# Kernel tuning notes

Hardware: AMD Instinct MI355X
Metric: run time of the kernel (lower is better)

The kernel has to match this reference:

```python
import jax, jax.numpy as jnp
import numpy as np

HID = 100

def _make_params(key):
    dims = [(2, HID), (HID, HID), (HID, HID), (HID, HID), (HID, 2)]
    params = {}
    for i, (fan_in, fan_out) in enumerate(dims):
        k1, k2, key = jax.random.split(key, 3)
        bound = 1.0 / np.sqrt(fan_in)
        params[f"W{i+1}"] = jax.random.uniform(k1, (fan_out, fan_in), jnp.float32, -bound, bound)
        params[f"b{i+1}"] = jax.random.uniform(k2, (fan_out,), jnp.float32, -bound, bound)
    return params

def setup_inputs() -> dict:
    key = jax.random.key(0)
    kx, kt, kp = jax.random.split(key, 3)
    N = 262144
    inp = {
        "x": jax.random.normal(kx, (N, 1), jnp.float32),
        "t": jax.random.uniform(kt, (N, 1), jnp.float32),
    }
    inp.update(_make_params(kp))
    return inp

def reference(x, t, W1, b1, W2, b2, W3, b3, W4, b4, W5, b5):
    hidden = [(W1, b1), (W2, b2), (W3, b3), (W4, b4)]

    def u(xs, ts):  # scalar xs, ts -> [2] = (u_r, u_i)
        h = jnp.stack([xs, ts])
        for W, b in hidden:
            h = jnp.tanh(W @ h + b)
        return W5 @ h + b5

    u_t = jax.jacfwd(u, argnums=1)          # [2]: (u_t_r, u_t_i)
    u_x = jax.jacfwd(u, argnums=0)          # [2]
    u_xx = jax.jacfwd(u_x, argnums=0)       # [2]: (u_xx_r, u_xx_i)

    def per_point(xs, ts):
        return u(xs, ts), u_t(xs, ts), u_xx(xs, ts)

    U, Ut, Uxx = jax.vmap(per_point)(x[:, 0], t[:, 0])  # each [N, 2]

    u_r, u_i = U[:, 0:1], U[:, 1:2]
    u_t_r, u_t_i = Ut[:, 0:1], Ut[:, 1:2]
    u_xx_r, u_xx_i = Uxx[:, 0:1], Uxx[:, 1:2]

    mag2 = u_r * u_r + u_i * u_i
    f_r = -u_t_i + 0.5 * u_xx_r + mag2 * u_r
    f_i = u_t_r + 0.5 * u_xx_i + mag2 * u_i
    return f_r, f_i
```

## Files before the change

### kernel.cpp

```cpp
#include <hip/hip_runtime.h>


using half8 = __attribute__((ext_vector_type(8))) _Float16;
using half4 = __attribute__((ext_vector_type(4))) _Float16;
using f32x4 = __attribute__((ext_vector_type(4))) float;

#define LW      44800
#define ZOFF    134400
#define STGOFF  134416
#define STGW    2304
#define PLANEB  1152
#define SMEM_BYTES 152848

union U8 { uint4 u; half8 h; };
union U4 { uint2 u; half4 h; };

static __device__ __forceinline__ float fast_tanh(float z) {
    float e = __expf(2.0f * z);
    return 1.0f - 2.0f * __builtin_amdgcn_rcpf(e + 1.0f);
}

static __device__ __forceinline__ void split2(float v, _Float16& h0, _Float16& h1) {
    h0 = (_Float16)v;
    h1 = (_Float16)((v - (float)h0) * 512.0f);
}

__global__ void prep_w(const float* __restrict__ W2, const float* __restrict__ W3,
                       const float* __restrict__ W4, unsigned short* __restrict__ ws) {
    int bid = blockIdx.x;
    int l = bid / 28, rem = bid % 28, kt = rem / 7, jt = rem % 7;
    const float* W = (l == 0) ? W2 : (l == 1) ? W3 : W4;
    int lane = threadIdx.x;
    int c = lane & 15, q = lane >> 4;
    int j = 16 * jt + c;
    if (kt < 3) {
        for (int s = 0; s < 2; ++s)
            for (int i = 0; i < 8; ++i) {
                int k = 32 * kt + 8 * q + i;
                float w = (j < 100) ? W[j * 100 + k] : 0.0f;
                _Float16 h0 = (_Float16)w;
                _Float16 val = (s == 0) ? h0 : (_Float16)((w - (float)h0) * 512.0f);
                ws[(l*LW + kt*14336 + jt*2048 + s*1024 + lane*16 + i*2) >> 1] =
                    __builtin_bit_cast(unsigned short, val);
            }
    } else if (lane < 16) {
        for (int s = 0; s < 2; ++s)
            for (int i = 0; i < 4; ++i) {
                int k = 96 + i;
                float w = (j < 100) ? W[j * 100 + k] : 0.0f;
                _Float16 h0 = (_Float16)w;
                _Float16 val = (s == 0) ? h0 : (_Float16)((w - (float)h0) * 512.0f);
                ws[(l*LW + 43008 + jt*256 + s*128 + lane*8 + i*2) >> 1] =
                    __builtin_bit_cast(unsigned short, val);
            }
    }
}

__global__ void __launch_bounds__(512, 2) pinn_mfma(
    const float* __restrict__ x,  const float* __restrict__ t,
    const float* __restrict__ W1, const float* __restrict__ b1,
    const float* __restrict__ b2, const float* __restrict__ b3,
    const float* __restrict__ b4,
    const float* __restrict__ W5, const float* __restrict__ b5,
    const char* __restrict__ ws, float* __restrict__ out,
    int N, int nchunks)
{
    extern __shared__ char smem[];
    const int tid  = threadIdx.x;
    const int w    = tid >> 6;
    const int lane = tid & 63;
    const int c15  = lane & 15;
    const int q    = lane >> 4;

    for (int it = 0; it < 17; ++it) {
        int idx = tid + it * 512;
        if (idx < 8400) ((uint4*)smem)[idx] = ((const uint4*)ws)[idx];
    }
    if (tid < 4) *(unsigned*)(smem + ZOFF + tid * 4) = 0u;
    __syncthreads();

    char* stg = smem + STGOFF + w * STGW;

    half8 a0[3], a1[3];
    half4 a0t,   a1t;
    f32x4 c0[7], c1[7];

    for (int chunk = blockIdx.x; chunk < nchunks; chunk += gridDim.x) {
        const int colbase = chunk * 128 + w * 16;

        {
            int col = colbase + c15;
            int pt = col >> 2, ch = col & 3;
            float xv = x[pt], tv = t[pt];
            #pragma unroll
            for (int kt = 0; kt < 3; ++kt) {
                half8 v0, v1;
                #pragma unroll
                for (int i = 0; i < 8; ++i) {
                    int j = 32 * kt + 8 * q + i;
                    float w0 = W1[2*j], w1 = W1[2*j+1], bb = b1[j];
                    float p = fmaf(w0, xv, fmaf(w1, tv, bb));
                    float a = fast_tanh(p);
                    float s = 1.0f - a * a;
                    float v = (ch == 0) ? a : (ch == 1) ? s * w1
                             : (ch == 2) ? s * w0 : -2.0f * a * s * w0 * w0;
                    _Float16 h0, h1; split2(v, h0, h1);
                    v0[i] = h0; v1[i] = h1;
                }
                a0[kt] = v0; a1[kt] = v1;
            }
            half4 t0 = {0, 0, 0, 0}, t1 = {0, 0, 0, 0};
            if (q == 0) {
                #pragma unroll
                for (int i = 0; i < 4; ++i) {
                    int j = 96 + i;
                    float w0 = W1[2*j], w1 = W1[2*j+1], bb = b1[j];
                    float p = fmaf(w0, xv, fmaf(w1, tv, bb));
                    float a = fast_tanh(p);
                    float s = 1.0f - a * a;
                    float v = (ch == 0) ? a : (ch == 1) ? s * w1
                             : (ch == 2) ? s * w0 : -2.0f * a * s * w0 * w0;
                    _Float16 h0, h1; split2(v, h0, h1);
                    t0[i] = h0; t1[i] = h1;
                }
            }
            a0t = t0; a1t = t1;
        }

        for (int l = 0; l < 3; ++l) {
            const char* WL = smem + l * LW;
            const float* BL = (l == 0) ? b2 : (l == 1) ? b3 : b4;

            #pragma unroll
            for (int jt = 0; jt < 7; ++jt) {
                c0[jt] = (f32x4){0.f, 0.f, 0.f, 0.f};
                c1[jt] = (f32x4){0.f, 0.f, 0.f, 0.f};
            }

            #pragma unroll
            for (int kt = 0; kt < 3; ++kt)
                #pragma unroll
                for (int jt = 0; jt < 7; ++jt) {
                    U8 b0u, b1u;
                    b0u.u = *(const uint4*)(WL + kt*14336 + jt*2048 + lane*16);
                    b1u.u = *(const uint4*)(WL + kt*14336 + jt*2048 + 1024 + lane*16);
                    c0[jt] = __builtin_amdgcn_mfma_f32_16x16x32_f16(a0[kt], b0u.h, c0[jt], 0, 0, 0);
                    c1[jt] = __builtin_amdgcn_mfma_f32_16x16x32_f16(a0[kt], b1u.h, c1[jt], 0, 0, 0);
                    c1[jt] = __builtin_amdgcn_mfma_f32_16x16x32_f16(a1[kt], b0u.h, c1[jt], 0, 0, 0);
                }
            #pragma unroll
            for (int jt = 0; jt < 7; ++jt) {
                int toff  = (lane < 16) ? (l*LW + 43008 + jt*256 + lane*8) : ZOFF;
                int toff1 = (lane < 16) ? (toff + 128) : ZOFF;
                U4 b0u, b1u;
                b0u.u = *(const uint2*)(smem + toff);
                b1u.u = *(const uint2*)(smem + toff1);
                c0[jt] = __builtin_amdgcn_mfma_f32_16x16x16f16(a0t, b0u.h, c0[jt], 0, 0, 0);
                c1[jt] = __builtin_amdgcn_mfma_f32_16x16x16f16(a0t, b1u.h, c1[jt], 0, 0, 0);
                c1[jt] = __builtin_amdgcn_mfma_f32_16x16x16f16(a1t, b0u.h, c1[jt], 0, 0, 0);
            }

            if (l < 2) {
                #pragma unroll
                for (int kc = 0; kc < 4; ++kc) {
                    int njt = (kc < 3) ? 2 : 1;
                    #pragma unroll
                    for (int jj = 0; jj < 2; ++jj) {
                        if (jj >= njt) continue;
                        int jt = 2 * kc + jj;
                        int kk = 16 * jj + c15;
                        int j  = 16 * jt + c15;
                        float bj = BL[(j < 100) ? j : 99];
                        float z0 = c0[jt][0] + c1[jt][0] * (1.0f/512.0f) + bj;
                        float z1 = c0[jt][1] + c1[jt][1] * (1.0f/512.0f);
                        float z2 = c0[jt][2] + c1[jt][2] * (1.0f/512.0f);
                        float z3 = c0[jt][3] + c1[jt][3] * (1.0f/512.0f);
                        float a = fast_tanh(z0);
                        float s = 1.0f - a * a;
                        float v[4];
                        v[0] = a; v[1] = s * z1; v[2] = s * z2;
                        v[3] = fmaf(-2.0f * a * s * z2, z2, s * z3);
                        #pragma unroll
                        for (int r = 0; r < 4; ++r) {
                            _Float16 h0, h1; split2(v[r], h0, h1);
                            _Float16* bp = (_Float16*)(stg) + (4 * q + r) * 36 + kk;
                            bp[0]   = h0;
                            bp[576] = h1;
                        }
                    }
                    if (kc < 3) {
                        const char* rb = stg + c15 * 72 + 16 * q;
                        U8 u;
                        uint2 L, H;
                        L = *(const uint2*)(rb);              H = *(const uint2*)(rb + 8);
                        u.u = (uint4){L.x, L.y, H.x, H.y};    a0[kc] = u.h;
                        L = *(const uint2*)(rb + PLANEB);     H = *(const uint2*)(rb + PLANEB + 8);
                        u.u = (uint4){L.x, L.y, H.x, H.y};    a1[kc] = u.h;
                    } else {
                        U4 u;
                        if (q == 0) {
                            const char* rb = stg + c15 * 72;
                            u.u = *(const uint2*)(rb);            a0t = u.h;
                            u.u = *(const uint2*)(rb + PLANEB);   a1t = u.h;
                        } else {
                            a0t = (half4){0,0,0,0}; a1t = (half4){0,0,0,0};
                        }
                    }
                }
            } else {
                float p00 = 0.f, p01 = 0.f, p03 = 0.f;
                float p10 = 0.f, p11 = 0.f, p13 = 0.f;
                #pragma unroll
                for (int jt = 0; jt < 7; ++jt) {
                    int j = 16 * jt + c15;
                    int j2 = (j < 100) ? j : 99;
                    float m = (j < 100) ? 1.0f : 0.0f;
                    float bj = BL[j2];
                    float w50 = W5[j2] * m, w51 = W5[100 + j2] * m;
                    float z0 = c0[jt][0] + c1[jt][0] * (1.0f/512.0f) + bj;
                    float z1 = c0[jt][1] + c1[jt][1] * (1.0f/512.0f);
                    float z2 = c0[jt][2] + c1[jt][2] * (1.0f/512.0f);
                    float z3 = c0[jt][3] + c1[jt][3] * (1.0f/512.0f);
                    float a = fast_tanh(z0);
                    float s = 1.0f - a * a;
                    float v0 = a, v1 = s * z1;
                    float v3 = fmaf(-2.0f * a * s * z2, z2, s * z3);
                    p00 = fmaf(w50, v0, p00);
                    p01 = fmaf(w50, v1, p01);
                    p03 = fmaf(w50, v3, p03);
                    p10 = fmaf(w51, v0, p10);
                    p11 = fmaf(w51, v1, p11);
                    p13 = fmaf(w51, v3, p13);
                }
                #pragma unroll
                for (int m = 1; m <= 8; m <<= 1) {
                    p00 += __shfl_xor(p00, m, 64);
                    p01 += __shfl_xor(p01, m, 64);
                    p03 += __shfl_xor(p03, m, 64);
                    p10 += __shfl_xor(p10, m, 64);
                    p11 += __shfl_xor(p11, m, 64);
                    p13 += __shfl_xor(p13, m, 64);
                }
                if (c15 == 0) {
                    float ur = p00 + b5[0], ui = p10 + b5[1];
                    float mag2 = ur * ur + ui * ui;
                    float fr = fmaf(mag2, ur, fmaf(0.5f, p03, -p11));
                    float fi = fmaf(mag2, ui, fmaf(0.5f, p13,  p01));
                    int pt = chunk * 32 + w * 4 + q;
                    out[pt]     = fr;
                    out[N + pt] = fi;
                }
            }
        }
    }
}

extern "C" void kernel_launch(void* const* d_in, const int* in_sizes, int n_in,
                              void* d_out, int out_size, void* d_ws, size_t ws_size,
                              hipStream_t stream) {
    const float* x  = (const float*)d_in[0];
    const float* t  = (const float*)d_in[1];
    const float* W1 = (const float*)d_in[2];
    const float* b1 = (const float*)d_in[3];
    const float* W2 = (const float*)d_in[4];
    const float* b2 = (const float*)d_in[5];
    const float* W3 = (const float*)d_in[6];
    const float* b3 = (const float*)d_in[7];
    const float* W4 = (const float*)d_in[8];
    const float* b4 = (const float*)d_in[9];
    const float* W5 = (const float*)d_in[10];
    const float* b5 = (const float*)d_in[11];
    float* out = (float*)d_out;
    const int N = in_sizes[0];
    const int nchunks = N / 32;

    (void)hipFuncSetAttribute((const void*)pinn_mfma,
                              hipFuncAttributeMaxDynamicSharedMemorySize, SMEM_BYTES);

    prep_w<<<84, 64, 0, stream>>>(W2, W3, W4, (unsigned short*)d_ws);
    pinn_mfma<<<256, 512, SMEM_BYTES, stream>>>(x, t, W1, b1, b2, b3, b4, W5, b5,
                                                (const char*)d_ws, out, N, nchunks);
}
```

Measured before the change: 465.7 us.

## Process two M-tiles per wave to reuse LDS weight fragments across MFMAs

Each wave now handles 32 columns (two 16-column M tiles) per chunk instead of 16, so each B-fragment loaded from LDS feeds twice as many MFMAs. The staging buffer row stride grows from 36 to 40 halves, which allows single 16-byte LDS reads in place of paired 8-byte reads. Chunk count halves and bounds guards are added for partial chunks. The cost is doubled accumulator and A-fragment register pressure, which may reduce occupancy or cause spills.

```diff
diff --git a/kernel.cpp b/kernel.cpp
--- a/kernel.cpp
+++ b/kernel.cpp
@@ -8,9 +8,9 @@
 #define LW      44800
 #define ZOFF    134400
 #define STGOFF  134416
-#define STGW    2304
-#define PLANEB  1152
-#define SMEM_BYTES 152848
+#define STGW    2560
+#define PLANEB  1280
+#define SMEM_BYTES 154896
 
 union U8 { uint4 u; half8 h; };
 union U4 { uint2 u; half4 h; };
@@ -81,17 +81,19 @@
 
     char* stg = smem + STGOFF + w * STGW;
 
-    half8 a0[3], a1[3];
-    half4 a0t,   a1t;
-    f32x4 c0[7], c1[7];
+    half8 a0[2][3], a1[2][3];
+    half4 a0t[2],   a1t[2];
+    f32x4 c0[7][2], c1[7][2];
 
     for (int chunk = blockIdx.x; chunk < nchunks; chunk += gridDim.x) {
-        const int colbase = chunk * 128 + w * 16;
-
-        {
-            int col = colbase + c15;
+        const int colbase = chunk * 256 + w * 32;
+
+        #pragma unroll
+        for (int mt = 0; mt < 2; ++mt) {
+            int col = colbase + 16 * mt + c15;
             int pt = col >> 2, ch = col & 3;
-            float xv = x[pt], tv = t[pt];
+            int ptc = (pt < N) ? pt : (N - 1);
+            float xv = x[ptc], tv = t[ptc];
             #pragma unroll
             for (int kt = 0; kt < 3; ++kt) {
                 half8 v0, v1;
@@ -107,7 +109,7 @@
                     _Float16 h0, h1; split2(v, h0, h1);
                     v0[i] = h0; v1[i] = h1;
                 }
-                a0[kt] = v0; a1[kt] = v1;
+                a0[mt][kt] = v0; a1[mt][kt] = v1;
             }
             half4 t0 = {0, 0, 0, 0}, t1 = {0, 0, 0, 0};
             if (q == 0) {
@@ -124,7 +126,7 @@
                     t0[i] = h0; t1[i] = h1;
                 }
             }
-            a0t = t0; a1t = t1;
+            a0t[mt] = t0; a1t[mt] = t1;
         }
 
         for (int l = 0; l < 3; ++l) {
@@ -132,10 +134,12 @@
             const float* BL = (l == 0) ? b2 : (l == 1) ? b3 : b4;
 
             #pragma unroll
-            for (int jt = 0; jt < 7; ++jt) {
-                c0[jt] = (f32x4){0.f, 0.f, 0.f, 0.f};
-                c1[jt] = (f32x4){0.f, 0.f, 0.f, 0.f};
-            }
+            for (int jt = 0; jt < 7; ++jt)
+                #pragma unroll
+                for (int mt = 0; mt < 2; ++mt) {
+                    c0[jt][mt] = (f32x4){0.f, 0.f, 0.f, 0.f};
+                    c1[jt][mt] = (f32x4){0.f, 0.f, 0.f, 0.f};
+                }
 
             #pragma unroll
             for (int kt = 0; kt < 3; ++kt)
@@ -144,9 +148,12 @@
                     U8 b0u, b1u;
                     b0u.u = *(const uint4*)(WL + kt*14336 + jt*2048 + lane*16);
                     b1u.u = *(const uint4*)(WL + kt*14336 + jt*2048 + 1024 + lane*16);
-                    c0[jt] = __builtin_amdgcn_mfma_f32_16x16x32_f16(a0[kt], b0u.h, c0[jt], 0, 0, 0);
-                    c1[jt] = __builtin_amdgcn_mfma_f32_16x16x32_f16(a0[kt], b1u.h, c1[jt], 0, 0, 0);
-                    c1[jt] = __builtin_amdgcn_mfma_f32_16x16x32_f16(a1[kt], b0u.h, c1[jt], 0, 0, 0);
+                    #pragma unroll
+                    for (int mt = 0; mt < 2; ++mt) {
+                        c0[jt][mt] = __builtin_amdgcn_mfma_f32_16x16x32_f16(a0[mt][kt], b0u.h, c0[jt][mt], 0, 0, 0);
+                        c1[jt][mt] = __builtin_amdgcn_mfma_f32_16x16x32_f16(a0[mt][kt], b1u.h, c1[jt][mt], 0, 0, 0);
+                        c1[jt][mt] = __builtin_amdgcn_mfma_f32_16x16x32_f16(a1[mt][kt], b0u.h, c1[jt][mt], 0, 0, 0);
+                    }
                 }
             #pragma unroll
             for (int jt = 0; jt < 7; ++jt) {
@@ -155,9 +162,12 @@
                 U4 b0u, b1u;
                 b0u.u = *(const uint2*)(smem + toff);
                 b1u.u = *(const uint2*)(smem + toff1);
-                c0[jt] = __builtin_amdgcn_mfma_f32_16x16x16f16(a0t, b0u.h, c0[jt], 0, 0, 0);
-                c1[jt] = __builtin_amdgcn_mfma_f32_16x16x16f16(a0t, b1u.h, c1[jt], 0, 0, 0);
-                c1[jt] = __builtin_amdgcn_mfma_f32_16x16x16f16(a1t, b0u.h, c1[jt], 0, 0, 0);
+                #pragma unroll
+                for (int mt = 0; mt < 2; ++mt) {
+                    c0[jt][mt] = __builtin_amdgcn_mfma_f32_16x16x16f16(a0t[mt], b0u.h, c0[jt][mt], 0, 0, 0);
+                    c1[jt][mt] = __builtin_amdgcn_mfma_f32_16x16x16f16(a0t[mt], b1u.h, c1[jt][mt], 0, 0, 0);
+                    c1[jt][mt] = __builtin_amdgcn_mfma_f32_16x16x16f16(a1t[mt], b0u.h, c1[jt][mt], 0, 0, 0);
+                }
             }
 
             if (l < 2) {
@@ -165,90 +175,93 @@
                 for (int kc = 0; kc < 4; ++kc) {
                     int njt = (kc < 3) ? 2 : 1;
                     #pragma unroll
-                    for (int jj = 0; jj < 2; ++jj) {
-                        if (jj >= njt) continue;
-                        int jt = 2 * kc + jj;
-                        int kk = 16 * jj + c15;
-                        int j  = 16 * jt + c15;
-                        float bj = BL[(j < 100) ? j : 99];
-                        float z0 = c0[jt][0] + c1[jt][0] * (1.0f/512.0f) + bj;
-                        float z1 = c0[jt][1] + c1[jt][1] * (1.0f/512.0f);
-                        float z2 = c0[jt][2] + c1[jt][2] * (1.0f/512.0f);
-                        float z3 = c0[jt][3] + c1[jt][3] * (1.0f/512.0f);
+                    for (int mtt = 0; mtt < 2; ++mtt) {
+                        #pragma unroll
+                        for (int jj = 0; jj < 2; ++jj) {
+                            if (jj >= njt) continue;
+                            int jt = 2 * kc + jj;
+                            int kk = 16 * jj + c15;
+                            int j  = 16 * jt + c15;
+                            float bj = BL[(j < 100) ? j : 99];
+                            float z0 = c0[jt][mtt][0] + c1[jt][mtt][0] * (1.0f/512.0f) + bj;
+                            float z1 = c0[jt][mtt][1] + c1[jt][mtt][1] * (1.0f/512.0f);
+                            float z2 = c0[jt][mtt][2] + c1[jt][mtt][2] * (1.0f/512.0f);
+                            float z3 = c0[jt][mtt][3] + c1[jt][mtt][3] * (1.0f/512.0f);
+                            float a = fast_tanh(z0);
+                            float s = 1.0f - a * a;
+                            float v[4];
+                            v[0] = a; v[1] = s * z1; v[2] = s * z2;
+                            v[3] = fmaf(-2.0f * a * s * z2, z2, s * z3);
+                            #pragma unroll
+                            for (int r = 0; r < 4; ++r) {
+                                _Float16 h0, h1; split2(v[r], h0, h1);
+                                _Float16* bp = (_Float16*)(stg) + (4 * q + r) * 40 + kk;
+                                bp[0]   = h0;
+                                bp[640] = h1;
+                            }
+                        }
+                        if (kc < 3) {
+                            const char* rb = stg + c15 * 80 + 16 * q;
+                            U8 u;
+                            u.u = *(const uint4*)(rb);            a0[mtt][kc] = u.h;
+                            u.u = *(const uint4*)(rb + PLANEB);   a1[mtt][kc] = u.h;
+                        } else {
+                            U4 u;
+                            if (q == 0) {
+                                const char* rb = stg + c15 * 80;
+                                u.u = *(const uint2*)(rb);            a0t[mtt] = u.h;
+                                u.u = *(const uint2*)(rb + PLANEB);   a1t[mtt] = u.h;
+                            } else {
+                                a0t[mtt] = (half4){0,0,0,0}; a1t[mtt] = (half4){0,0,0,0};
+                            }
+                        }
+                    }
+                }
+            } else {
+                #pragma unroll
+                for (int mt = 0; mt < 2; ++mt) {
+                    float p00 = 0.f, p01 = 0.f, p03 = 0.f;
+                    float p10 = 0.f, p11 = 0.f, p13 = 0.f;
+                    #pragma unroll
+                    for (int jt = 0; jt < 7; ++jt) {
+                        int j = 16 * jt + c15;
+                        int j2 = (j < 100) ? j : 99;
+                        float m = (j < 100) ? 1.0f : 0.0f;
+                        float bj = BL[j2];
+                        float w50 = W5[j2] * m, w51 = W5[100 + j2] * m;
+                        float z0 = c0[jt][mt][0] + c1[jt][mt][0] * (1.0f/512.0f) + bj;
+                        float z1 = c0[jt][mt][1] + c1[jt][mt][1] * (1.0f/512.0f);
+                        float z2 = c0[jt][mt][2] + c1[jt][mt][2] * (1.0f/512.0f);
+                        float z3 = c0[jt][mt][3] + c1[jt][mt][3] * (1.0f/512.0f);
                         float a = fast_tanh(z0);
                         float s = 1.0f - a * a;
-                        float v[4];
-                        v[0] = a; v[1] = s * z1; v[2] = s * z2;
-                        v[3] = fmaf(-2.0f * a * s * z2, z2, s * z3);
-                        #pragma unroll
-                        for (int r = 0; r < 4; ++r) {
-                            _Float16 h0, h1; split2(v[r], h0, h1);
-                            _Float16* bp = (_Float16*)(stg) + (4 * q + r) * 36 + kk;
-                            bp[0]   = h0;
-                            bp[576] = h1;
-                        }
-                    }
-                    if (kc < 3) {
-                        const char* rb = stg + c15 * 72 + 16 * q;
-                        U8 u;
-                        uint2 L, H;
-                        L = *(const uint2*)(rb);              H = *(const uint2*)(rb + 8);
-                        u.u = (uint4){L.x, L.y, H.x, H.y};    a0[kc] = u.h;
-                        L = *(const uint2*)(rb + PLANEB);     H = *(const uint2*)(rb + PLANEB + 8);
-                        u.u = (uint4){L.x, L.y, H.x, H.y};    a1[kc] = u.h;
-                    } else {
-                        U4 u;
-                        if (q == 0) {
-                            const char* rb = stg + c15 * 72;
-                            u.u = *(const uint2*)(rb);            a0t = u.h;
-                            u.u = *(const uint2*)(rb + PLANEB);   a1t = u.h;
-                        } else {
-                            a0t = (half4){0,0,0,0}; a1t = (half4){0,0,0,0};
-                        }
-                    }
-                }
-            } else {
-                float p00 = 0.f, p01 = 0.f, p03 = 0.f;
-                float p10 = 0.f, p11 = 0.f, p13 = 0.f;
-                #pragma unroll
-                for (int jt = 0; jt < 7; ++jt) {
-                    int j = 16 * jt + c15;
-                    int j2 = (j < 100) ? j : 99;
-                    float m = (j < 100) ? 1.0f : 0.0f;
-                    float bj = BL[j2];
-                    float w50 = W5[j2] * m, w51 = W5[100 + j2] * m;
-                    float z0 = c0[jt][0] + c1[jt][0] * (1.0f/512.0f) + bj;
-                    float z1 = c0[jt][1] + c1[jt][1] * (1.0f/512.0f);
-                    float z2 = c0[jt][2] + c1[jt][2] * (1.0f/512.0f);
-                    float z3 = c0[jt][3] + c1[jt][3] * (1.0f/512.0f);
-                    float a = fast_tanh(z0);
-                    float s = 1.0f - a * a;
-                    float v0 = a, v1 = s * z1;
-                    float v3 = fmaf(-2.0f * a * s * z2, z2, s * z3);
-                    p00 = fmaf(w50, v0, p00);
-                    p01 = fmaf(w50, v1, p01);
-                    p03 = fmaf(w50, v3, p03);
-                    p10 = fmaf(w51, v0, p10);
-                    p11 = fmaf(w51, v1, p11);
-                    p13 = fmaf(w51, v3, p13);
-                }
-                #pragma unroll
-                for (int m = 1; m <= 8; m <<= 1) {
-                    p00 += __shfl_xor(p00, m, 64);
-                    p01 += __shfl_xor(p01, m, 64);
-                    p03 += __shfl_xor(p03, m, 64);
-                    p10 += __shfl_xor(p10, m, 64);
-                    p11 += __shfl_xor(p11, m, 64);
-                    p13 += __shfl_xor(p13, m, 64);
-                }
-                if (c15 == 0) {
-                    float ur = p00 + b5[0], ui = p10 + b5[1];
-                    float mag2 = ur * ur + ui * ui;
-                    float fr = fmaf(mag2, ur, fmaf(0.5f, p03, -p11));
-                    float fi = fmaf(mag2, ui, fmaf(0.5f, p13,  p01));
-                    int pt = chunk * 32 + w * 4 + q;
-                    out[pt]     = fr;
-                    out[N + pt] = fi;
+                        float v0 = a, v1 = s * z1;
+                        float v3 = fmaf(-2.0f * a * s * z2, z2, s * z3);
+                        p00 = fmaf(w50, v0, p00);
+                        p01 = fmaf(w50, v1, p01);
+                        p03 = fmaf(w50, v3, p03);
+                        p10 = fmaf(w51, v0, p10);
+                        p11 = fmaf(w51, v1, p11);
+                        p13 = fmaf(w51, v3, p13);
+                    }
+                    #pragma unroll
+                    for (int m = 1; m <= 8; m <<= 1) {
+                        p00 += __shfl_xor(p00, m, 64);
+                        p01 += __shfl_xor(p01, m, 64);
+                        p03 += __shfl_xor(p03, m, 64);
+                        p10 += __shfl_xor(p10, m, 64);
+                        p11 += __shfl_xor(p11, m, 64);
+                        p13 += __shfl_xor(p13, m, 64);
+                    }
+                    int pt = chunk * 64 + w * 8 + 4 * mt + q;
+                    if (c15 == 0 && pt < N) {
+                        float ur = p00 + b5[0], ui = p10 + b5[1];
+                        float mag2 = ur * ur + ui * ui;
+                        float fr = fmaf(mag2, ur, fmaf(0.5f, p03, -p11));
+                        float fi = fmaf(mag2, ui, fmaf(0.5f, p13,  p01));
+                        out[pt]     = fr;
+                        out[N + pt] = fi;
+                    }
                 }
             }
         }
@@ -272,7 +285,7 @@
     const float* b5 = (const float*)d_in[11];
     float* out = (float*)d_out;
     const int N = in_sizes[0];
-    const int nchunks = N / 32;
+    const int nchunks = (N + 63) / 64;
 
     (void)hipFuncSetAttribute((const void*)pinn_mfma,
                               hipFuncAttributeMaxDynamicSharedMemorySize, SMEM_BYTES);
```

Measured after the change: 472.6 us. Within noise of the previous version (+1.5%).
